# Kernel optimization log

Hardware: AMD Instinct MI355X
Metric: run time of the kernel (lower is better)

The kernel has to match this reference:

```python
import jax, jax.numpy as jnp
import numpy as np

B, C, H, W = 256, 1024, 7, 7
D_HID, N_CLS = 768, 5

def setup_inputs() -> dict:
    key = jax.random.key(0)
    k1, k2, k3, k4, k5 = jax.random.split(key, 5)
    flat = C * H * W  # 50176
    return {
        "features": jax.random.normal(k1, (B, C, H, W), dtype=jnp.float32),
        "W1": jax.random.normal(k2, (D_HID, flat), dtype=jnp.float32) * 0.02,
        "b1": jax.random.normal(k3, (D_HID,), dtype=jnp.float32) * 0.02,
        "W2": jax.random.normal(k4, (N_CLS, D_HID), dtype=jnp.float32) * 0.02,
        "b2": jax.random.normal(k5, (N_CLS,), dtype=jnp.float32) * 0.02,
    }

def reference(features, W1, b1, W2, b2):
    # PCAM: per-(batch, channel) global max over spatial dims, broadcast-multiplied
    # back onto the feature map. Replaces the torch Python double loop with one
    # fused reduce-max + elementwise multiply.
    ch_max = jnp.max(features, axis=(2, 3), keepdims=True)  # [B, C, 1, 1]
    pcams = features * ch_max                               # [B, C, H, W]
    flat = pcams.reshape(pcams.shape[0], -1)                # [B, C*H*W]
    h = jax.nn.relu(flat @ W1.T + b1)                       # [B, 768]
    logits = h @ W2.T + b2                                  # [B, num_classes]
    return (logits, features)
```

## Files before the change

kernel.cpp:

```cpp
#include <hip/hip_runtime.h>
#include <hip/hip_bf16.h>

#define B_SZ   256
#define C_SZ   1024
#define HW     49
#define KDIM   50176
#define DHID   768
#define NCLS   5

typedef __bf16 bf16x8 __attribute__((ext_vector_type(8)));
typedef float  f32x4  __attribute__((ext_vector_type(4)));

#define GLOAD_LDS16(gsrc, ldst) \
  __builtin_amdgcn_global_load_lds((__attribute__((address_space(1))) void*)(gsrc), \
                                   (__attribute__((address_space(3))) void*)(ldst), 16, 0, 0)

__global__ __launch_bounds__(256) void pcam_kernel(const float* __restrict__ feat,
                                                   float* __restrict__ feat_out,
                                                   __bf16* __restrict__ pcam) {
  __shared__ float sv[1568];
  __shared__ float smax[32];
  const int tid = threadIdx.x;
  const size_t base = (size_t)blockIdx.x * 1568;

  const float4* src4 = (const float4*)(feat + base);
  float4* dst4 = (float4*)(feat_out + base);
  #pragma unroll
  for (int i = 0; i < 2; ++i) {
    int idx = tid + i * 256;
    if (idx < 392) {
      float4 v = src4[idx];
      dst4[idx] = v;
      ((float4*)sv)[idx] = v;
    }
  }
  __syncthreads();

  {
    const int r = tid >> 3, p = tid & 7;
    float mx = -INFINITY;
    for (int i = p; i < HW; i += 8) mx = fmaxf(mx, sv[r * HW + i]);
    #pragma unroll
    for (int off = 1; off < 8; off <<= 1) mx = fmaxf(mx, __shfl_xor(mx, off));
    if (p == 0) smax[r] = mx;
  }
  __syncthreads();

  for (int i = tid; i < 1568; i += 256) {
    int r = (i * 1338) >> 16;
    float v = sv[i] * smax[r];
    pcam[base + i] = (__bf16)v;
  }
}

#define BM 256
#define BN 256
#define BK 64
#define NT 3
#define KSPLIT 85
#define KSTEPS 784

__global__ __launch_bounds__(512, 2) void gemm1_kernel(const __bf16* __restrict__ pcam,
                                                       const float* __restrict__ W1,
                                                       float* __restrict__ h_part) {
  __shared__ __bf16 Asm[BM * BK];
  __shared__ float  Bsm[BN * BK];

  const int tid  = threadIdx.x;
  const int lane = tid & 63;
  const int w    = tid >> 6;
  const int wm   = w >> 2;
  const int wn   = w & 3;
  const int n0   = blockIdx.x * BN;
  const int ks   = blockIdx.y;
  const int s0   = (ks * KSTEPS) / KSPLIT;
  const int s1   = ((ks + 1) * KSTEPS) / KSPLIT;

  unsigned a_off[4];
  #pragma unroll
  for (int it = 0; it < 4; ++it) {
    const unsigned ug = it * 512 + tid;
    const unsigned m  = ug >> 3;
    a_off[it] = m * (unsigned)KDIM + (((ug & 7) ^ (m & 7)) * 8u);
  }
  unsigned b_off[8];
  #pragma unroll
  for (int it = 0; it < 8; ++it) {
    const unsigned ug = it * 512 + tid;
    const unsigned r  = ug >> 4;
    const unsigned up = ug & 15;
    b_off[it] = (unsigned)(n0 + r) * KDIM + ((((up >> 1) ^ (r & 7)) * 8u) + ((up & 1) * 4u));
  }

  f32x4 acc[8][4];
  #pragma unroll
  for (int i = 0; i < 8; ++i)
    #pragma unroll
    for (int j = 0; j < 4; ++j) acc[i][j] = f32x4{0.f, 0.f, 0.f, 0.f};

  const int j_ = lane >> 4;
  const int c_ = lane & 15;

  for (int s = s0; s < s1; ++s) {
    const unsigned ka = (unsigned)s * BK;
    #pragma unroll
    for (int it = 0; it < 4; ++it)
      GLOAD_LDS16(pcam + a_off[it] + ka, (char*)Asm + it * 8192 + w * 1024);
    #pragma unroll
    for (int it = 0; it < 8; ++it)
      GLOAD_LDS16(W1 + b_off[it] + ka, (char*)Bsm + it * 8192 + w * 1024);
    __syncthreads();

    #pragma unroll
    for (int ksub = 0; ksub < 2; ++ksub) {
      const int u = ksub * 4 + j_;
      bf16x8 af[8];
      #pragma unroll
      for (int i = 0; i < 8; ++i) {
        const int m = wm * 128 + i * 16 + c_;
        af[i] = *(const bf16x8*)((const char*)Asm + m * 128 + ((u ^ (m & 7)) << 4));
      }
      #pragma unroll
      for (int jf = 0; jf < 4; ++jf) {
        const int r  = wn * 64 + jf * 16 + c_;
        const int gp = u ^ (r & 7);
        const f32x4 v0 = *(const f32x4*)((const char*)Bsm + r * 256 + gp * 32);
        const f32x4 v1 = *(const f32x4*)((const char*)Bsm + r * 256 + gp * 32 + 16);
        bf16x8 bfr;
        bfr[0] = (__bf16)v0[0]; bfr[1] = (__bf16)v0[1];
        bfr[2] = (__bf16)v0[2]; bfr[3] = (__bf16)v0[3];
        bfr[4] = (__bf16)v1[0]; bfr[5] = (__bf16)v1[1];
        bfr[6] = (__bf16)v1[2]; bfr[7] = (__bf16)v1[3];
        #pragma unroll
        for (int i = 0; i < 8; ++i)
          acc[i][jf] = __builtin_amdgcn_mfma_f32_16x16x32_bf16(af[i], bfr, acc[i][jf], 0, 0, 0);
      }
    }
    __syncthreads();
  }

  float* out = h_part + (size_t)ks * DHID * B_SZ;
  #pragma unroll
  for (int i = 0; i < 8; ++i) {
    const int mb = wm * 128 + i * 16 + j_ * 4;
    #pragma unroll
    for (int jf = 0; jf < 4; ++jf) {
      const int n = n0 + wn * 64 + jf * 16 + c_;
      *(f32x4*)(out + (size_t)n * B_SZ + mb) = acc[i][jf];
    }
  }
}

__global__ __launch_bounds__(256) void reduce_kernel(const float* __restrict__ h_part,
                                                     const float* __restrict__ b1,
                                                     float* __restrict__ h) {
  const int n = blockIdx.x;
  const int m = threadIdx.x;
  float s = 0.f;
  #pragma unroll 5
  for (int ks = 0; ks < KSPLIT; ++ks)
    s += h_part[((size_t)ks * DHID + n) * B_SZ + m];
  float v = s + b1[n];
  h[(size_t)m * DHID + n] = v > 0.f ? v : 0.f;
}

__global__ __launch_bounds__(64) void head_kernel(const float* __restrict__ h,
                                                  const float* __restrict__ W2,
                                                  const float* __restrict__ b2,
                                                  float* __restrict__ logits) {
  const int m = blockIdx.x;
  const int lane = threadIdx.x;
  float hv[12];
  #pragma unroll
  for (int j = 0; j < 12; ++j) hv[j] = h[(size_t)m * DHID + j * 64 + lane];
  #pragma unroll
  for (int c = 0; c < NCLS; ++c) {
    float s = 0.f;
    #pragma unroll
    for (int j = 0; j < 12; ++j) s += hv[j] * W2[c * DHID + j * 64 + lane];
    #pragma unroll
    for (int off = 32; off > 0; off >>= 1) s += __shfl_xor(s, off);
    if (lane == 0) logits[m * NCLS + c] = s + b2[c];
  }
}

extern "C" void kernel_launch(void* const* d_in, const int* in_sizes, int n_in,
                              void* d_out, int out_size, void* d_ws, size_t ws_size,
                              hipStream_t stream) {
  const float* feat = (const float*)d_in[0];
  const float* W1   = (const float*)d_in[1];
  const float* b1   = (const float*)d_in[2];
  const float* W2   = (const float*)d_in[3];
  const float* b2   = (const float*)d_in[4];

  float* logits   = (float*)d_out;
  float* feat_out = (float*)d_out + (size_t)B_SZ * NCLS;

  char* ws = (char*)d_ws;
  __bf16* pcam   = (__bf16*)ws;
  float*  h_part = (float*)(ws + (size_t)B_SZ * KDIM * 2);
  float*  h      = (float*)(ws + (size_t)B_SZ * KDIM * 2
                               + (size_t)KSPLIT * DHID * B_SZ * 4);

  pcam_kernel<<<(B_SZ * C_SZ) / 32, 256, 0, stream>>>(feat, feat_out, pcam);
  gemm1_kernel<<<dim3(NT, KSPLIT), 512, 0, stream>>>(pcam, W1, h_part);
  reduce_kernel<<<DHID, 256, 0, stream>>>(h_part, b1, h);
  head_kernel<<<B_SZ, 64, 0, stream>>>(h, W2, b2, logits);
}
```

Before: 106.6 us.

## Restructure GEMM1: register-staged double-buffered A tile, direct W1 fragment loads

The GEMM tiling changes from 256x256 tiles with an 85-way K split to 256x128 tiles with a 42-way K split. Each wave now owns 16 output columns and loads its W1 fragment straight from global memory into registers, dropping the LDS staging of W1. The pcam A tile is prefetched into registers and written to a double-buffered LDS slot, so there is one barrier per step and global loads overlap compute. This trades the async global-to-LDS loads for register staging and uncoalesced per-lane W1 reads, and it shrinks the partial-sum buffer that the reduce kernel must read.

```diff
diff --git a/kernel.cpp b/kernel.cpp
--- a/kernel.cpp
+++ b/kernel.cpp
@@ -11,9 +11,11 @@
 typedef __bf16 bf16x8 __attribute__((ext_vector_type(8)));
 typedef float  f32x4  __attribute__((ext_vector_type(4)));
 
-#define GLOAD_LDS16(gsrc, ldst) \
-  __builtin_amdgcn_global_load_lds((__attribute__((address_space(1))) void*)(gsrc), \
-                                   (__attribute__((address_space(3))) void*)(ldst), 16, 0, 0)
+#define BARRIER() do { \
+    asm volatile("s_waitcnt lgkmcnt(0)" ::: "memory"); \
+    __builtin_amdgcn_s_barrier(); \
+    asm volatile("" ::: "memory"); \
+  } while (0)
 
 __global__ __launch_bounds__(256) void pcam_kernel(const float* __restrict__ feat,
                                                    float* __restrict__ feat_out,
@@ -54,101 +56,98 @@
 }
 
 #define BM 256
-#define BN 256
-#define BK 64
-#define NT 3
-#define KSPLIT 85
+#define BN 128
+#define KC 64
+#define NT 6
+#define KSPLIT 42
 #define KSTEPS 784
 
 __global__ __launch_bounds__(512, 2) void gemm1_kernel(const __bf16* __restrict__ pcam,
                                                        const float* __restrict__ W1,
                                                        float* __restrict__ h_part) {
-  __shared__ __bf16 Asm[BM * BK];
-  __shared__ float  Bsm[BN * BK];
+  __shared__ __bf16 Asm[2][BM * KC];
 
   const int tid  = threadIdx.x;
   const int lane = tid & 63;
   const int w    = tid >> 6;
-  const int wm   = w >> 2;
-  const int wn   = w & 3;
   const int n0   = blockIdx.x * BN;
   const int ks   = blockIdx.y;
   const int s0   = (ks * KSTEPS) / KSPLIT;
   const int s1   = ((ks + 1) * KSTEPS) / KSPLIT;
 
+  const float* bbase = W1 + (size_t)(n0 + w * 16 + (lane & 15)) * KDIM + (lane >> 4) * 8;
+
   unsigned a_off[4];
+  int      a_lds[4];
   #pragma unroll
   for (int it = 0; it < 4; ++it) {
     const unsigned ug = it * 512 + tid;
     const unsigned m  = ug >> 3;
-    a_off[it] = m * (unsigned)KDIM + (((ug & 7) ^ (m & 7)) * 8u);
-  }
-  unsigned b_off[8];
-  #pragma unroll
-  for (int it = 0; it < 8; ++it) {
-    const unsigned ug = it * 512 + tid;
-    const unsigned r  = ug >> 4;
-    const unsigned up = ug & 15;
-    b_off[it] = (unsigned)(n0 + r) * KDIM + ((((up >> 1) ^ (r & 7)) * 8u) + ((up & 1) * 4u));
-  }
-
-  f32x4 acc[8][4];
-  #pragma unroll
-  for (int i = 0; i < 8; ++i)
-    #pragma unroll
-    for (int j = 0; j < 4; ++j) acc[i][j] = f32x4{0.f, 0.f, 0.f, 0.f};
-
-  const int j_ = lane >> 4;
-  const int c_ = lane & 15;
+    const unsigned u  = ug & 7;
+    a_off[it] = m * (unsigned)KDIM + ((u ^ (m & 7)) * 8u);
+    a_lds[it] = (int)(ug * 8);
+  }
+
+  f32x4 acc[16];
+  #pragma unroll
+  for (int i = 0; i < 16; ++i) acc[i] = f32x4{0.f, 0.f, 0.f, 0.f};
+
+  bf16x8 ar[4];
+
+#define LOAD_A(s) do { \
+    _Pragma("unroll") \
+    for (int it = 0; it < 4; ++it) \
+      ar[it] = *(const bf16x8*)(pcam + a_off[it] + (unsigned)(s) * KC); \
+  } while (0)
+
+#define WRITE_A(bi) do { \
+    _Pragma("unroll") \
+    for (int it = 0; it < 4; ++it) \
+      *(bf16x8*)(&Asm[bi][a_lds[it]]) = ar[it]; \
+  } while (0)
+
+#define COMPUTE(bi, s) do { \
+    _Pragma("unroll") \
+    for (int ksub = 0; ksub < 2; ++ksub) { \
+      const f32x4 v0 = *(const f32x4*)(bbase + (size_t)(s) * KC + ksub * 32); \
+      const f32x4 v1 = *(const f32x4*)(bbase + (size_t)(s) * KC + ksub * 32 + 4); \
+      bf16x8 bfr; \
+      bfr[0] = (__bf16)v0[0]; bfr[1] = (__bf16)v0[1]; \
+      bfr[2] = (__bf16)v0[2]; bfr[3] = (__bf16)v0[3]; \
+      bfr[4] = (__bf16)v1[0]; bfr[5] = (__bf16)v1[1]; \
+      bfr[6] = (__bf16)v1[2]; bfr[7] = (__bf16)v1[3]; \
+      const int u = ksub * 4 + (lane >> 4); \
+      _Pragma("unroll") \
+      for (int i = 0; i < 16; ++i) { \
+        const int m = i * 16 + (lane & 15); \
+        const bf16x8 af = *(const bf16x8*)((const char*)Asm[bi] + m * 128 + ((u ^ (m & 7)) << 4)); \
+        acc[i] = __builtin_amdgcn_mfma_f32_16x16x32_bf16(af, bfr, acc[i], 0, 0, 0); \
+      } \
+    } \
+  } while (0)
+
+  LOAD_A(s0);
+  WRITE_A(0);
+  BARRIER();
 
   for (int s = s0; s < s1; ++s) {
-    const unsigned ka = (unsigned)s * BK;
-    #pragma unroll
-    for (int it = 0; it < 4; ++it)
-      GLOAD_LDS16(pcam + a_off[it] + ka, (char*)Asm + it * 8192 + w * 1024);
-    #pragma unroll
-    for (int it = 0; it < 8; ++it)
-      GLOAD_LDS16(W1 + b_off[it] + ka, (char*)Bsm + it * 8192 + w * 1024);
-    __syncthreads();
-
-    #pragma unroll
-    for (int ksub = 0; ksub < 2; ++ksub) {
-      const int u = ksub * 4 + j_;
-      bf16x8 af[8];
-      #pragma unroll
-      for (int i = 0; i < 8; ++i) {
-        const int m = wm * 128 + i * 16 + c_;
-        af[i] = *(const bf16x8*)((const char*)Asm + m * 128 + ((u ^ (m & 7)) << 4));
-      }
-      #pragma unroll
-      for (int jf = 0; jf < 4; ++jf) {
-        const int r  = wn * 64 + jf * 16 + c_;
-        const int gp = u ^ (r & 7);
-        const f32x4 v0 = *(const f32x4*)((const char*)Bsm + r * 256 + gp * 32);
-        const f32x4 v1 = *(const f32x4*)((const char*)Bsm + r * 256 + gp * 32 + 16);
-        bf16x8 bfr;
-        bfr[0] = (__bf16)v0[0]; bfr[1] = (__bf16)v0[1];
-        bfr[2] = (__bf16)v0[2]; bfr[3] = (__bf16)v0[3];
-        bfr[4] = (__bf16)v1[0]; bfr[5] = (__bf16)v1[1];
-        bfr[6] = (__bf16)v1[2]; bfr[7] = (__bf16)v1[3];
-        #pragma unroll
-        for (int i = 0; i < 8; ++i)
-          acc[i][jf] = __builtin_amdgcn_mfma_f32_16x16x32_bf16(af[i], bfr, acc[i][jf], 0, 0, 0);
-      }
-    }
-    __syncthreads();
+    const int cur = (s - s0) & 1;
+    if (s + 1 < s1) LOAD_A(s + 1);
+    COMPUTE(cur, s);
+    if (s + 1 < s1) WRITE_A(cur ^ 1);
+    BARRIER();
   }
 
   float* out = h_part + (size_t)ks * DHID * B_SZ;
-  #pragma unroll
-  for (int i = 0; i < 8; ++i) {
-    const int mb = wm * 128 + i * 16 + j_ * 4;
-    #pragma unroll
-    for (int jf = 0; jf < 4; ++jf) {
-      const int n = n0 + wn * 64 + jf * 16 + c_;
-      *(f32x4*)(out + (size_t)n * B_SZ + mb) = acc[i][jf];
-    }
-  }
+  const int n = n0 + w * 16 + (lane & 15);
+  #pragma unroll
+  for (int i = 0; i < 16; ++i) {
+    const int mb = i * 16 + (lane >> 4) * 4;
+    *(f32x4*)(out + (size_t)n * B_SZ + mb) = acc[i];
+  }
+#undef LOAD_A
+#undef WRITE_A
+#undef COMPUTE
 }
 
 __global__ __launch_bounds__(256) void reduce_kernel(const float* __restrict__ h_part,
@@ -157,7 +156,7 @@
   const int n = blockIdx.x;
   const int m = threadIdx.x;
   float s = 0.f;
-  #pragma unroll 5
+  #pragma unroll 6
   for (int ks = 0; ks < KSPLIT; ++ks)
     s += h_part[((size_t)ks * DHID + n) * B_SZ + m];
   float v = s + b1[n];
```

Result: faster. 103.9 us (-2.6%).
